# Optimization experiments

Hardware: AMD Instinct MI355X
Metric: run time of the kernel (lower is better)

The kernel has to match this reference:

```python
import jax, jax.numpy as jnp
import numpy as np

N_HEADS = 16
HIDDEN = 1024
HEAD_DIM = 64
BSZ = 4
SEQ = 1024
SCALE = HEAD_DIM ** -0.5


def setup_inputs() -> dict:
    key = jax.random.key(0)
    k_x, k_q, k_k, k_v, k_o = jax.random.split(key, 5)
    s = HIDDEN ** -0.5
    return {
        "x": jax.random.normal(k_x, (BSZ, SEQ, HIDDEN), dtype=jnp.float32),
        # torch nn.Linear weights: shape (out_features, in_features)
        "wq": jax.random.normal(k_q, (N_HEADS * HEAD_DIM, HIDDEN), dtype=jnp.float32) * s,
        "wk": jax.random.normal(k_k, (N_HEADS * HEAD_DIM, HIDDEN), dtype=jnp.float32) * s,
        "wv": jax.random.normal(k_v, (N_HEADS * HEAD_DIM, HIDDEN), dtype=jnp.float32) * s,
        "wo": jax.random.normal(k_o, (HIDDEN, N_HEADS * HEAD_DIM), dtype=jnp.float32) * s,
    }


def reference(x, wq, wk, wv, wo):
    bsz, seqlen, _ = x.shape
    xq = jnp.einsum("bsh,oh->bso", x, wq)  # (b, s, n_heads*head_dim)
    xk = jnp.einsum("bsh,oh->bso", x, wk)
    xv = jnp.einsum("bsh,oh->bso", x, wv)
    # Faithful to the original: raw view to (b, n_heads, s, head_dim), NO transpose
    xq = xq.reshape(bsz, N_HEADS, seqlen, HEAD_DIM)
    xk = xk.reshape(bsz, N_HEADS, seqlen, HEAD_DIM)
    xv = xv.reshape(bsz, N_HEADS, seqlen, HEAD_DIM)
    scores = jnp.einsum("bhid,bhjd->bhij", xq, xk) * SCALE
    scores = jax.nn.softmax(scores, axis=-1)
    out = jnp.einsum("bhij,bhjd->bhid", scores, xv)
    out = out.reshape(bsz, seqlen, N_HEADS * HEAD_DIM)  # raw view, faithful
    return jnp.einsum("bso,ho->bsh", out, wo)
```

## Files before the change

kernel.cpp:

```cpp
#include <hip/hip_runtime.h>
#include <hip/hip_bf16.h>

typedef __hip_bfloat16 bf16;
typedef __attribute__((ext_vector_type(8))) short short8;
typedef __attribute__((ext_vector_type(4))) short short4v;
typedef __attribute__((ext_vector_type(4))) float f32x4;


__device__ __forceinline__ short f2b(float x) {
    bf16 h = __float2bfloat16(x);
    return *reinterpret_cast<short*>(&h);
}
__device__ __forceinline__ f32x4 zero4() {
    f32x4 z; z[0] = 0.f; z[1] = 0.f; z[2] = 0.f; z[3] = 0.f; return z;
}
__device__ __forceinline__ void gl_lds16(const void* g, void* l) {
    __builtin_amdgcn_global_load_lds(
        (const __attribute__((address_space(1))) void*)g,
        (__attribute__((address_space(3))) void*)l, 16, 0, 0);
}

__global__ __launch_bounds__(256) void convert_in(const float* __restrict__ w0,
                                                  const float* __restrict__ w1,
                                                  const float* __restrict__ w2,
                                                  const float* __restrict__ w3,
                                                  const float* __restrict__ x,
                                                  bf16* __restrict__ Wb,
                                                  bf16* __restrict__ Xb) {
    const int y = blockIdx.y;
    const float* s;
    bf16* d;
    if (y < 4) {
        s = (y == 0) ? w0 : (y == 1) ? w1 : (y == 2) ? w2 : w3;
        d = Wb + (size_t)y * 1048576;
    } else {
        s = x + (size_t)(y - 4) * 1048576;
        d = Xb + (size_t)(y - 4) * 1048576;
    }
    const int i = (blockIdx.x * 256 + threadIdx.x) * 4;
    const float4 v = *(const float4*)(s + i);
    short4v o;
    o[0] = f2b(v.x); o[1] = f2b(v.y); o[2] = f2b(v.z); o[3] = f2b(v.w);
    *(short4v*)(d + i) = o;
}

__global__ __launch_bounds__(256) void gemm_qkv(const bf16* __restrict__ Xb,
                                                const bf16* __restrict__ Wb,
                                                bf16* __restrict__ QK,
                                                bf16* __restrict__ VT) {
    __shared__ __align__(16) bf16 As[128 * 32];
    __shared__ __align__(16) bf16 Bs[128 * 32];

    const int tid  = threadIdx.x;
    const int wave = tid >> 6;
    const int lane = tid & 63;
    const int z    = blockIdx.z;
    const int bm   = blockIdx.x * 128, bn = blockIdx.y * 128;
    const bf16* Bsrc = Wb + (size_t)z * 1048576;

    const int f0 = wave * 2048 + lane * 16, f1 = f0 + 1024;
    const char* gA0 = (const char*)(Xb + (size_t)(bm + (f0 >> 6)) * 1024) + (f0 & 63);
    const char* gA1 = (const char*)(Xb + (size_t)(bm + (f1 >> 6)) * 1024) + (f1 & 63);
    const char* gB0 = (const char*)(Bsrc + (size_t)(bn + (f0 >> 6)) * 1024) + (f0 & 63);
    const char* gB1 = (const char*)(Bsrc + (size_t)(bn + (f1 >> 6)) * 1024) + (f1 & 63);
    char* lA0 = (char*)As + wave * 2048;      char* lA1 = lA0 + 1024;
    char* lB0 = (char*)Bs + wave * 2048;      char* lB1 = lB0 + 1024;

    f32x4 acc[4][4];
#pragma unroll
    for (int i = 0; i < 4; i++)
#pragma unroll
        for (int j = 0; j < 4; j++) acc[i][j] = zero4();

    const int mrow = ((wave >> 1) * 64) + (lane & 15);
    const int nrow = ((wave & 1) * 64) + (lane & 15);
    const int kcol = (lane >> 4) * 8;

    for (int k0 = 0; k0 < 1024; k0 += 32) {
        __syncthreads();
        gl_lds16(gA0 + (size_t)k0 * 2, lA0);
        gl_lds16(gA1 + (size_t)k0 * 2, lA1);
        gl_lds16(gB0 + (size_t)k0 * 2, lB0);
        gl_lds16(gB1 + (size_t)k0 * 2, lB1);
        __syncthreads();
        short8 af[4], bfr[4];
#pragma unroll
        for (int i = 0; i < 4; i++)
            af[i] = *(const short8*)&As[(mrow + i * 16) * 32 + kcol];
#pragma unroll
        for (int j = 0; j < 4; j++)
            bfr[j] = *(const short8*)&Bs[(nrow + j * 16) * 32 + kcol];
#pragma unroll
        for (int i = 0; i < 4; i++)
#pragma unroll
            for (int j = 0; j < 4; j++)
                acc[i][j] = __builtin_amdgcn_mfma_f32_16x16x32_bf16(
                    af[i], bfr[j], acc[i][j], 0, 0, 0);
    }

    const int erow = bm + (wave >> 1) * 64 + (lane >> 4) * 4;
    const int ecol = bn + (wave & 1) * 64 + (lane & 15);
    if (z < 2) {
        bf16* C = QK + (size_t)z * 4194304;
#pragma unroll
        for (int i = 0; i < 4; i++)
#pragma unroll
            for (int j = 0; j < 4; j++)
#pragma unroll
                for (int r = 0; r < 4; r++)
                    C[(size_t)(erow + i * 16 + r) * 1024 + (ecol + j * 16)] =
                        __float2bfloat16(acc[i][j][r]);
    } else {
#pragma unroll
        for (int i = 0; i < 4; i++)
#pragma unroll
            for (int j = 0; j < 4; j++) {
                const int o  = ecol + j * 16;
                const int d  = o & 63;
                const int oh = o >> 6;
#pragma unroll
                for (int r = 0; r < 4; r++) {
                    const int rr = erow + i * 16 + r;
                    VT[(size_t)(rr >> 6) * 65536 + d * 1024 +
                       ((rr & 63) * 16 + oh)] = __float2bfloat16(acc[i][j][r]);
                }
            }
    }
}

__global__ __launch_bounds__(256, 4) void gemm_out(const bf16* __restrict__ A,
                                                   const bf16* __restrict__ B,
                                                   float* __restrict__ C) {
    __shared__ __align__(16) bf16 As[2][64 * 32];
    __shared__ __align__(16) bf16 Bs[2][64 * 32];

    const int tid  = threadIdx.x;
    const int wave = tid >> 6;
    const int lane = tid & 63;
    const int bm   = blockIdx.x * 64, bn = blockIdx.y * 64;

    const int fA = tid * 16;
    const char* gA = (const char*)(A + (size_t)(bm + (fA >> 6)) * 1024) + (fA & 63);
    const char* gB = (const char*)(B + (size_t)(bn + (fA >> 6)) * 1024) + (fA & 63);
    char* Ab = (char*)As;
    char* Bb = (char*)Bs;

    f32x4 acc[2][2];
#pragma unroll
    for (int i = 0; i < 2; i++)
#pragma unroll
        for (int j = 0; j < 2; j++) acc[i][j] = zero4();

    const int mrow = ((wave >> 1) * 32) + (lane & 15);
    const int nrow = ((wave & 1) * 32) + (lane & 15);
    const int kcol = (lane >> 4) * 8;

    gl_lds16(gA, Ab + fA);
    gl_lds16(gB, Bb + fA);

    for (int kt = 0; kt < 32; ++kt) {
        const int p  = (kt & 1) * 4096;
        const int pn = 4096 - p;
        const int kn = (kt < 31) ? kt + 1 : 0;
        asm volatile("" ::: "memory");
        __builtin_amdgcn_s_barrier();
        gl_lds16(gA + (size_t)kn * 64, Ab + pn + fA);
        gl_lds16(gB + (size_t)kn * 64, Bb + pn + fA);
        asm volatile("s_waitcnt vmcnt(2)" ::: "memory");
        __builtin_amdgcn_s_barrier();
        asm volatile("" ::: "memory");

        short8 af[2], bfr[2];
#pragma unroll
        for (int i = 0; i < 2; i++)
            af[i] = *(const short8*)(Ab + p + (((mrow + i * 16) * 32 + kcol) << 1));
#pragma unroll
        for (int j = 0; j < 2; j++)
            bfr[j] = *(const short8*)(Bb + p + (((nrow + j * 16) * 32 + kcol) << 1));
#pragma unroll
        for (int i = 0; i < 2; i++)
#pragma unroll
            for (int j = 0; j < 2; j++)
                acc[i][j] = __builtin_amdgcn_mfma_f32_16x16x32_bf16(
                    af[i], bfr[j], acc[i][j], 0, 0, 0);
    }
    asm volatile("s_waitcnt vmcnt(0)" ::: "memory");

    const int erow = bm + (wave >> 1) * 32 + (lane >> 4) * 4;
    const int ecol = bn + (wave & 1) * 32 + (lane & 15);
#pragma unroll
    for (int i = 0; i < 2; i++)
#pragma unroll
        for (int j = 0; j < 2; j++)
#pragma unroll
            for (int r = 0; r < 4; r++)
                C[(size_t)(erow + i * 16 + r) * 1024 + (ecol + j * 16)] =
                    acc[i][j][r];
}

__global__ __launch_bounds__(256) void attn(bf16* __restrict__ QO,
                                            const bf16* __restrict__ K,
                                            const bf16* __restrict__ VT) {
    __shared__ __align__(16) bf16 Ks[2][64 * 64];
    __shared__ __align__(16) bf16 Vs[2][64 * 64];
    __shared__ __align__(16) unsigned int Ps2[128 * 32];

    const int tid  = threadIdx.x;
    const int wave = tid >> 6;
    const int lane = tid & 63;
    const int lg   = lane >> 4;
    const int li   = lane & 15;
    const int xsw  = (li & 7) << 2;

    const int bid  = blockIdx.x;
    const int head = ((bid & 7) << 3) | ((bid >> 3) & 7);
    const int qt   = bid >> 6;
    bf16* Qh = QO + (size_t)head * 65536 + qt * 8192;
    const char* Khb  = (const char*)(K + (size_t)head * 65536);
    const char* VThb = (const char*)(VT + (size_t)head * 65536);

    short8 qf[2][2];
#pragma unroll
    for (int i = 0; i < 2; i++)
#pragma unroll
        for (int ks = 0; ks < 2; ks++)
            qf[i][ks] = *(const short8*)&Qh[(wave * 32 + i * 16 + li) * 64 +
                                            ks * 32 + lg * 8];

    f32x4 o_acc[2][4];
    float lp2[2];
#pragma unroll
    for (int i = 0; i < 2; i++) {
#pragma unroll
        for (int j = 0; j < 4; j++) o_acc[i][j] = zero4();
        lp2[i] = 0.f;
    }

    unsigned int* pb[2];
#pragma unroll
    for (int i = 0; i < 2; i++)
        pb[i] = Ps2 + (wave * 32 + i * 16 + li) * 32;

    const int fs0 = wave * 2048 + lane * 16, fs1 = fs0 + 1024;
    char* KsB = (char*)Ks;
    char* VsB = (char*)Vs;
    const char* gV0 = VThb + (size_t)(fs0 >> 7) * 2048 + (fs0 & 127);
    const char* gV1 = VThb + (size_t)(fs1 >> 7) * 2048 + (fs1 & 127);

    gl_lds16(Khb + fs0, KsB + fs0);
    gl_lds16(Khb + fs1, KsB + fs1);
    gl_lds16(gV0, VsB + fs0);
    gl_lds16(gV1, VsB + fs1);

    for (int jt = 0; jt < 16; jt++) {
        const int p  = (jt & 1) * 8192;
        const int pn = 8192 - p;
        const int jn = (jt < 15) ? jt + 1 : 15;
        asm volatile("" ::: "memory");
        __builtin_amdgcn_s_barrier();
        gl_lds16(Khb + (size_t)jn * 8192 + fs0, KsB + pn + fs0);
        gl_lds16(Khb + (size_t)jn * 8192 + fs1, KsB + pn + fs1);
        gl_lds16(gV0 + jn * 128, VsB + pn + fs0);
        gl_lds16(gV1 + jn * 128, VsB + pn + fs1);
        asm volatile("s_waitcnt vmcnt(4)" ::: "memory");
        __builtin_amdgcn_s_barrier();
        asm volatile("" ::: "memory");

        const bf16* Kc = (const bf16*)(KsB + p);
        const bf16* Vc = (const bf16*)(VsB + p);

        f32x4 s2[2][4];
#pragma unroll
        for (int i = 0; i < 2; i++)
#pragma unroll
            for (int j = 0; j < 4; j++) s2[i][j] = zero4();
#pragma unroll
        for (int j = 0; j < 4; j++)
#pragma unroll
            for (int ks = 0; ks < 2; ks++) {
                short8 kf = *(const short8*)&Kc[(j * 16 + li) * 64 + ks * 32 + lg * 8];
#pragma unroll
                for (int i = 0; i < 2; i++)
                    s2[i][j] = __builtin_amdgcn_mfma_f32_16x16x32_bf16(
                        kf, qf[i][ks], s2[i][j], 0, 0, 0);
            }

#pragma unroll
        for (int i = 0; i < 2; i++) {
            float ps = 0.f;
#pragma unroll
            for (int j = 0; j < 4; j++) {
                const float p0 = __expf(s2[i][j][0] * 0.125f);
                const float p1 = __expf(s2[i][j][1] * 0.125f);
                const float p2 = __expf(s2[i][j][2] * 0.125f);
                const float p3 = __expf(s2[i][j][3] * 0.125f);
                ps += (p0 + p1) + (p2 + p3);
                unsigned int w0, w1;
                asm("v_cvt_pk_bf16_f32 %0, %1, %2" : "=v"(w0) : "v"(p0), "v"(p1));
                asm("v_cvt_pk_bf16_f32 %0, %1, %2" : "=v"(w1) : "v"(p2), "v"(p3));
                *(unsigned long long*)(pb[i] + ((j * 8 + lg * 2) ^ xsw)) =
                    ((unsigned long long)w1 << 32) | w0;
            }
            lp2[i] += ps;
        }

#pragma unroll
        for (int ks = 0; ks < 2; ks++) {
            short8 pa[2];
#pragma unroll
            for (int i = 0; i < 2; i++)
                pa[i] = *(const short8*)(pb[i] + ((ks * 16 + lg * 4) ^ xsw));
#pragma unroll
            for (int jd = 0; jd < 4; jd++) {
                short8 vf = *(const short8*)&Vc[(jd * 16 + li) * 64 + ks * 32 + lg * 8];
#pragma unroll
                for (int i = 0; i < 2; i++)
                    o_acc[i][jd] = __builtin_amdgcn_mfma_f32_16x16x32_bf16(
                        pa[i], vf, o_acc[i][jd], 0, 0, 0);
            }
        }
    }
    asm volatile("s_waitcnt vmcnt(0)" ::: "memory");

#pragma unroll
    for (int i = 0; i < 2; i++) {
        float l = lp2[i];
        l += __shfl_xor(l, 16);
        l += __shfl_xor(l, 32);
#pragma unroll
        for (int r = 0; r < 4; r++) {
            const float lr = __shfl(l, (lane & 48) | (lg * 4 + r));
            const float inv = 1.f / lr;
#pragma unroll
            for (int jd = 0; jd < 4; jd++)
                Qh[(wave * 32 + i * 16 + lg * 4 + r) * 64 + jd * 16 + li] =
                    __float2bfloat16(o_acc[i][jd][r] * inv);
        }
    }
}

extern "C" void kernel_launch(void* const* d_in, const int* in_sizes, int n_in,
                              void* d_out, int out_size, void* d_ws, size_t ws_size,
                              hipStream_t stream) {
    const float* x  = (const float*)d_in[0];
    const float* wq = (const float*)d_in[1];
    const float* wk = (const float*)d_in[2];
    const float* wv = (const float*)d_in[3];
    const float* wo = (const float*)d_in[4];

    bf16* ws = (bf16*)d_ws;
    bf16* Wb = ws;
    bf16* QK = ws + 4194304;
    bf16* VT = ws + 12582912;
    bf16* Xb = (bf16*)d_out;

    convert_in<<<dim3(1024, 8), 256, 0, stream>>>(wq, wk, wv, wo, x, Wb, Xb);
    gemm_qkv<<<dim3(32, 8, 3), 256, 0, stream>>>(Xb, Wb, QK, VT);
    attn<<<512, 256, 0, stream>>>(QK, QK + 4194304, VT);
    gemm_out<<<dim3(64, 16), 256, 0, stream>>>(QK, Wb + 3145728, (float*)d_out);
}
```

Before: 177.9 us.

## Use two waves per block with 128x64 per-wave tiles in QKV GEMM

The QKV projection GEMM now runs 128 threads (2 waves) per block instead of 4, and each wave computes a 128x64 output tile (8x4 MFMA fragments) rather than 64x64. Each thread issues four global-to-LDS loads per operand per k-step. The aim is more MFMA work per LDS fragment load and fewer waves contending at each barrier. In exchange each thread holds twice the accumulator registers, and the total wave count in flight drops.

```diff
diff --git a/kernel.cpp b/kernel.cpp
--- a/kernel.cpp
+++ b/kernel.cpp
@@ -44,66 +44,69 @@
     *(short4v*)(d + i) = o;
 }
 
-__global__ __launch_bounds__(256) void gemm_qkv(const bf16* __restrict__ Xb,
-                                                const bf16* __restrict__ Wb,
-                                                bf16* __restrict__ QK,
-                                                bf16* __restrict__ VT) {
+__global__ __launch_bounds__(128, 2) void gemm_qkv(const bf16* __restrict__ Xb,
+                                                   const bf16* __restrict__ Wb,
+                                                   bf16* __restrict__ QK,
+                                                   bf16* __restrict__ VT) {
     __shared__ __align__(16) bf16 As[128 * 32];
     __shared__ __align__(16) bf16 Bs[128 * 32];
 
     const int tid  = threadIdx.x;
-    const int wave = tid >> 6;
+    const int w    = tid >> 6;
     const int lane = tid & 63;
+    const int li   = lane & 15;
+    const int lg   = lane >> 4;
     const int z    = blockIdx.z;
     const int bm   = blockIdx.x * 128, bn = blockIdx.y * 128;
     const bf16* Bsrc = Wb + (size_t)z * 1048576;
 
-    const int f0 = wave * 2048 + lane * 16, f1 = f0 + 1024;
-    const char* gA0 = (const char*)(Xb + (size_t)(bm + (f0 >> 6)) * 1024) + (f0 & 63);
-    const char* gA1 = (const char*)(Xb + (size_t)(bm + (f1 >> 6)) * 1024) + (f1 & 63);
-    const char* gB0 = (const char*)(Bsrc + (size_t)(bn + (f0 >> 6)) * 1024) + (f0 & 63);
-    const char* gB1 = (const char*)(Bsrc + (size_t)(bn + (f1 >> 6)) * 1024) + (f1 & 63);
-    char* lA0 = (char*)As + wave * 2048;      char* lA1 = lA0 + 1024;
-    char* lB0 = (char*)Bs + wave * 2048;      char* lB1 = lB0 + 1024;
-
-    f32x4 acc[4][4];
-#pragma unroll
-    for (int i = 0; i < 4; i++)
+    const char* gA[4]; const char* gB[4];
+    int lo[4];
+#pragma unroll
+    for (int c = 0; c < 4; c++) {
+        const int o = c * 2048 + tid * 16;
+        gA[c] = (const char*)(Xb   + (size_t)(bm + (o >> 6)) * 1024) + (o & 63);
+        gB[c] = (const char*)(Bsrc + (size_t)(bn + (o >> 6)) * 1024) + (o & 63);
+        lo[c] = o;
+    }
+
+    f32x4 acc[8][4];
+#pragma unroll
+    for (int i = 0; i < 8; i++)
 #pragma unroll
         for (int j = 0; j < 4; j++) acc[i][j] = zero4();
 
-    const int mrow = ((wave >> 1) * 64) + (lane & 15);
-    const int nrow = ((wave & 1) * 64) + (lane & 15);
-    const int kcol = (lane >> 4) * 8;
+    const int kcol = lg * 8;
 
     for (int k0 = 0; k0 < 1024; k0 += 32) {
         __syncthreads();
-        gl_lds16(gA0 + (size_t)k0 * 2, lA0);
-        gl_lds16(gA1 + (size_t)k0 * 2, lA1);
-        gl_lds16(gB0 + (size_t)k0 * 2, lB0);
-        gl_lds16(gB1 + (size_t)k0 * 2, lB1);
+#pragma unroll
+        for (int c = 0; c < 4; c++) {
+            gl_lds16(gA[c] + (size_t)k0 * 2, (char*)As + lo[c]);
+            gl_lds16(gB[c] + (size_t)k0 * 2, (char*)Bs + lo[c]);
+        }
         __syncthreads();
-        short8 af[4], bfr[4];
-#pragma unroll
-        for (int i = 0; i < 4; i++)
-            af[i] = *(const short8*)&As[(mrow + i * 16) * 32 + kcol];
+        short8 af[8], bfr[4];
+#pragma unroll
+        for (int i = 0; i < 8; i++)
+            af[i] = *(const short8*)&As[(i * 16 + li) * 32 + kcol];
 #pragma unroll
         for (int j = 0; j < 4; j++)
-            bfr[j] = *(const short8*)&Bs[(nrow + j * 16) * 32 + kcol];
-#pragma unroll
-        for (int i = 0; i < 4; i++)
+            bfr[j] = *(const short8*)&Bs[(w * 64 + j * 16 + li) * 32 + kcol];
+#pragma unroll
+        for (int i = 0; i < 8; i++)
 #pragma unroll
             for (int j = 0; j < 4; j++)
                 acc[i][j] = __builtin_amdgcn_mfma_f32_16x16x32_bf16(
                     af[i], bfr[j], acc[i][j], 0, 0, 0);
     }
 
-    const int erow = bm + (wave >> 1) * 64 + (lane >> 4) * 4;
-    const int ecol = bn + (wave & 1) * 64 + (lane & 15);
+    const int erow = bm + lg * 4;
+    const int ecol = bn + w * 64 + li;
     if (z < 2) {
         bf16* C = QK + (size_t)z * 4194304;
 #pragma unroll
-        for (int i = 0; i < 4; i++)
+        for (int i = 0; i < 8; i++)
 #pragma unroll
             for (int j = 0; j < 4; j++)
 #pragma unroll
@@ -112,7 +115,7 @@
                         __float2bfloat16(acc[i][j][r]);
     } else {
 #pragma unroll
-        for (int i = 0; i < 4; i++)
+        for (int i = 0; i < 8; i++)
 #pragma unroll
             for (int j = 0; j < 4; j++) {
                 const int o  = ecol + j * 16;
@@ -355,7 +358,7 @@
     bf16* Xb = (bf16*)d_out;
 
     convert_in<<<dim3(1024, 8), 256, 0, stream>>>(wq, wk, wv, wo, x, Wb, Xb);
-    gemm_qkv<<<dim3(32, 8, 3), 256, 0, stream>>>(Xb, Wb, QK, VT);
+    gemm_qkv<<<dim3(32, 8, 3), 128, 0, stream>>>(Xb, Wb, QK, VT);
     attn<<<512, 256, 0, stream>>>(QK, QK + 4194304, VT);
     gemm_out<<<dim3(64, 16), 256, 0, stream>>>(QK, Wb + 3145728, (float*)d_out);
 }
```

Measured after the change: 182.9 us. 1.03x slower.
